# Optimization experiments

Measured on AMD Instinct MI355X. Metric: run time of the kernel, lower is better.

Reference implementation:

```python
import jax, jax.numpy as jnp
import numpy as np

N = 50000
E = 800000
H = 96
NUM_IN = 11
PE_DIM = 24
NUM_OUT = 1
NUM_LAYERS = 4
NUM_GRAPHS = 256


def _linear_params(key, d_in, d_out):
    k1, k2 = jax.random.split(key)
    bound = 1.0 / np.sqrt(d_in)
    w = jax.random.uniform(k1, (d_in, d_out), jnp.float32, -bound, bound)
    b = jax.random.uniform(k2, (d_out,), jnp.float32, -bound, bound)
    return w, b


def setup_inputs() -> dict:
    key = jax.random.key(0)
    ks = jax.random.split(key, 32)
    x = jax.random.normal(ks[0], (N, NUM_IN), jnp.float32)
    pos = jax.random.normal(ks[1], (N, 3), jnp.float32)
    pe = jax.random.normal(ks[2], (N, PE_DIM), jnp.float32)
    edge_index = jax.random.randint(ks[3], (2, E), 0, N, jnp.int64)
    batch = jnp.sort(jax.random.randint(ks[4], (N,), 0, NUM_GRAPHS, jnp.int64))
    embed_w1, embed_b1 = _linear_params(ks[5], NUM_IN + PE_DIM, H)
    embed_w2, embed_b2 = _linear_params(ks[6], H, H)
    # per-layer stacked params
    msg_w1 = []; msg_b1 = []; msg_w2 = []; msg_b2 = []
    upd_w1 = []; upd_b1 = []; upd_w2 = []; upd_b2 = []
    for l in range(NUM_LAYERS):
        w, b = _linear_params(ks[7 + l], 2 * H + 1, H); msg_w1.append(w); msg_b1.append(b)
        w, b = _linear_params(ks[11 + l], H, H); msg_w2.append(w); msg_b2.append(b)
        w, b = _linear_params(ks[15 + l], 2 * H, H); upd_w1.append(w); upd_b1.append(b)
        w, b = _linear_params(ks[19 + l], H, H); upd_w2.append(w); upd_b2.append(b)
    pre_w1, pre_b1 = _linear_params(ks[23], H, H)
    pre_w2, pre_b2 = _linear_params(ks[24], H, H)
    ro_w1, ro_b1 = _linear_params(ks[25], H, H)
    ro_w2, ro_b2 = _linear_params(ks[26], H, NUM_OUT)
    return {
        'x': x, 'pos': pos, 'pe': pe, 'edge_index': edge_index, 'batch': batch,
        'embed_w1': embed_w1, 'embed_b1': embed_b1, 'embed_w2': embed_w2, 'embed_b2': embed_b2,
        'msg_w1': jnp.stack(msg_w1), 'msg_b1': jnp.stack(msg_b1),
        'msg_w2': jnp.stack(msg_w2), 'msg_b2': jnp.stack(msg_b2),
        'upd_w1': jnp.stack(upd_w1), 'upd_b1': jnp.stack(upd_b1),
        'upd_w2': jnp.stack(upd_w2), 'upd_b2': jnp.stack(upd_b2),
        'pre_w1': pre_w1, 'pre_b1': pre_b1, 'pre_w2': pre_w2, 'pre_b2': pre_b2,
        'ro_w1': ro_w1, 'ro_b1': ro_b1, 'ro_w2': ro_w2, 'ro_b2': ro_b2,
    }


def _egnn_forward(x, pos, pe, edge_index, batch,
                  embed_w1, embed_b1, embed_w2, embed_b2,
                  msg_w1, msg_b1, msg_w2, msg_b2,
                  upd_w1, upd_b1, upd_w2, upd_b2,
                  pre_w1, pre_b1, pre_w2, pre_b2,
                  ro_w1, ro_b1, ro_w2, ro_b2):
    silu = jax.nn.silu
    send, rec = edge_index[0], edge_index[1]
    h = jnp.concatenate([x, pe], axis=-1)
    h = silu(h @ embed_w1 + embed_b1) @ embed_w2 + embed_b2  # [N,H]
    dist = jnp.linalg.norm(pos[send] - pos[rec], axis=1)[:, None]  # [E,1]
    for l in range(NUM_LAYERS):
        state = jnp.concatenate([h[send], h[rec], dist], axis=1)  # [E,2H+1]
        msg = silu(silu(state @ msg_w1[l] + msg_b1[l]) @ msg_w2[l] + msg_b2[l])  # [E,H]
        aggr = jax.ops.segment_sum(msg, rec, num_segments=h.shape[0])  # [N,H]
        upd_in = jnp.concatenate([h, aggr], axis=1)
        update = silu(upd_in @ upd_w1[l] + upd_b1[l]) @ upd_w2[l] + upd_b2[l]
        h = h + update
    h = silu(h @ pre_w1 + pre_b1) @ pre_w2 + pre_b2
    pooled = jax.ops.segment_sum(h, batch, num_segments=NUM_GRAPHS)  # [G,H]
    out = silu(pooled @ ro_w1 + ro_b1) @ ro_w2 + ro_b2  # [G,1]
    return jnp.squeeze(out)


def reference(x, pos, pe, edge_index, batch,
              embed_w1, embed_b1, embed_w2, embed_b2,
              msg_w1, msg_b1, msg_w2, msg_b2,
              upd_w1, upd_b1, upd_w2, upd_b2,
              pre_w1, pre_b1, pre_w2, pre_b2,
              ro_w1, ro_b1, ro_w2, ro_b2):
    return _egnn_forward(x, pos, pe, edge_index, batch,
                         embed_w1, embed_b1, embed_w2, embed_b2,
                         msg_w1, msg_b1, msg_w2, msg_b2,
                         upd_w1, upd_b1, upd_w2, upd_b2,
                         pre_w1, pre_b1, pre_w2, pre_b2,
                         ro_w1, ro_b1, ro_w2, ro_b2)
```

## Files before the change

### kernel.cpp

```cpp
#include <hip/hip_runtime.h>
#include <hip/hip_bf16.h>

#define HDIM 96
#define TILE 128
#define NTILE 64

typedef __attribute__((ext_vector_type(8))) short  short8;
typedef __attribute__((ext_vector_type(4))) short  short4v;
typedef __attribute__((ext_vector_type(4))) float  float4v;
typedef __attribute__((ext_vector_type(2))) float  float2v;
typedef __attribute__((ext_vector_type(4))) unsigned int uint4v;
typedef __attribute__((ext_vector_type(2))) unsigned int uint2v;

static __device__ __forceinline__ short f2bf(float f){
    unsigned u = __float_as_uint(f);
    return (short)((u + 0x8000u) >> 16);
}
static __device__ __forceinline__ float bf2f(short s){
    unsigned u = ((unsigned)(unsigned short)s) << 16;
    return __uint_as_float(u);
}
static __device__ __forceinline__ float silu_f(float v){
    return v * __builtin_amdgcn_rcpf(1.0f + __expf(-v));
}
static __device__ __forceinline__ unsigned silu2_pack(float2v v){
    float e0 = __expf(-v[0]);
    float e1 = __expf(-v[1]);
    float2v ep = {e0, e1};
    const float2v one2 = {1.0f, 1.0f};
    ep += one2;
    float2v q = { __builtin_amdgcn_rcpf(ep[0]), __builtin_amdgcn_rcpf(ep[1]) };
    float2v res = v * q;
    unsigned pa = __float_as_uint(res[0]) + 0x8000u;
    unsigned pb = __float_as_uint(res[1]) + 0x8000u;
    return __builtin_amdgcn_perm(pb, pa, 0x07060302);
}

typedef __attribute__((address_space(1))) const unsigned int guint;
typedef __attribute__((address_space(3))) unsigned int luint;
static __device__ __forceinline__ void gload_lds16(const void* g, void* l){
    __builtin_amdgcn_global_load_lds((guint*)g, (luint*)l, 16, 0, 0);
}

struct SwJob { const float* src; int ck; int ks; int ksrc; };
struct SwTable { SwJob j[22]; };

__global__ __launch_bounds__(256) void swizzle_all(SwTable T, const float* __restrict__ msg_w1,
                                                   short* __restrict__ dst, short* __restrict__ dst2,
                                                   int total1, int total2,
                                                   float* __restrict__ aggrZ, float* __restrict__ pooledZ,
                                                   int* __restrict__ degZ, int nA, int nP, int nD){
    int gid = blockIdx.x*256 + threadIdx.x;
    if (gid < total1) {
        int ksg = gid / 3072;
        int e   = gid % 3072;
        const float* src = T.j[0].src; int k0 = 0, ksrc = 0;
        #pragma unroll
        for (int jj = 0; jj < 22; ++jj){
            int s = T.j[jj].ck;
            if (ksg >= s && ksg < s + T.j[jj].ks){ src = T.j[jj].src; k0 = (ksg - s)*32; ksrc = T.j[jj].ksrc; }
        }
        int nt   = e >> 9;
        int rem  = e & 511;
        int lane = rem >> 3;
        int jx   = rem & 7;
        int k = k0 + ((lane >> 4) << 3) + jx;
        int f = nt*16 + (lane & 15);
        float v = (k < ksrc) ? src[(size_t)k*HDIM + f] : 0.0f;
        dst[gid] = f2bf(v);
    } else if (gid < total1 + total2) {
        int g2 = gid - total1;
        int layer = g2 / 18432;
        int e     = g2 % 18432;
        int ksg = e / 6144;
        int rem = e % 6144;
        int nt   = rem >> 9;
        int r2   = rem & 511;
        int lane = r2 >> 3;
        int jx   = r2 & 7;
        int k = ksg*32 + ((lane >> 4) << 3) + jx;
        int f = nt*16 + (lane & 15);
        int row = (f < 96) ? k : (96 + k);
        int col = (f < 96) ? f : (f - 96);
        dst2[g2] = f2bf(msg_w1[(size_t)layer*193*96 + (size_t)row*96 + col]);
    } else {
        int gz = gid - total1 - total2;
        const float4v z = {0.f,0.f,0.f,0.f};
        if (gz < nA)                 ((float4v*)aggrZ)[gz] = z;
        else if (gz < nA + nP)       ((float4v*)pooledZ)[gz - nA] = z;
        else if (gz < nA + nP + nD)  ((float4v*)degZ)[gz - nA - nP] = z;
    }
}

__global__ __launch_bounds__(256) void hist_kernel(const int* __restrict__ rec, int* __restrict__ deg, int E){
    int e = blockIdx.x*256 + threadIdx.x;
    if (e < E) atomicAdd(&deg[rec[e]], 1);
}

__global__ __launch_bounds__(256) void scan_part(const int* __restrict__ deg, int* __restrict__ part, int N){
    __shared__ int red[256];
    const int t = threadIdx.x;
    int base = blockIdx.x*1024;
    int s = 0;
    #pragma unroll
    for (int j=0;j<4;j++){ int i = base + j*256 + t; s += (i<N)?deg[i]:0; }
    red[t]=s; __syncthreads();
    #pragma unroll
    for (int off=128; off>0; off>>=1){ if (t<off) red[t]+=red[t+off]; __syncthreads(); }
    if (t==0) part[blockIdx.x]=red[0];
}
__global__ __launch_bounds__(256) void scan_top(int* __restrict__ part, int nb){
    __shared__ int buf[256];
    const int t = threadIdx.x;
    int v = (t < nb) ? part[t] : 0;
    buf[t] = v;
    __syncthreads();
    #pragma unroll
    for (int off=1; off<256; off<<=1){
        int u = (t>=off)?buf[t-off]:0;
        __syncthreads();
        buf[t] += u;
        __syncthreads();
    }
    if (t < nb) part[t] = buf[t] - v;
}
__global__ __launch_bounds__(256) void scan_final(int* __restrict__ deg, const int* __restrict__ part,
                                                  int* __restrict__ cur, int N){
    __shared__ int tsum[256];
    const int t = threadIdx.x;
    int i0 = blockIdx.x*1024 + t*4;
    int a0 = (i0+0<N)?deg[i0+0]:0;
    int a1 = (i0+1<N)?deg[i0+1]:0;
    int a2 = (i0+2<N)?deg[i0+2]:0;
    int a3 = (i0+3<N)?deg[i0+3]:0;
    int s = a0+a1+a2+a3;
    tsum[t]=s; __syncthreads();
    #pragma unroll
    for (int off=1; off<256; off<<=1){
        int u = (t>=off)?tsum[t-off]:0;
        __syncthreads();
        tsum[t]+=u;
        __syncthreads();
    }
    int excl = tsum[t]-s + part[blockIdx.x];
    int e0 = excl, e1 = excl+a0, e2 = excl+a0+a1, e3 = excl+a0+a1+a2;
    if (i0+0<N){ cur[i0+0]=e0; if (a0>0 && (e0>>7)!=((e0+a0-1)>>7)) deg[i0+0]=a0|0x80000000; }
    if (i0+1<N){ cur[i0+1]=e1; if (a1>0 && (e1>>7)!=((e1+a1-1)>>7)) deg[i0+1]=a1|0x80000000; }
    if (i0+2<N){ cur[i0+2]=e2; if (a2>0 && (e2>>7)!=((e2+a2-1)>>7)) deg[i0+2]=a2|0x80000000; }
    if (i0+3<N){ cur[i0+3]=e3; if (a3>0 && (e3>>7)!=((e3+a3-1)>>7)) deg[i0+3]=a3|0x80000000; }
}

__global__ __launch_bounds__(256) void scatter_kernel(
    const int* __restrict__ send, const int* __restrict__ rec, const float* __restrict__ pos,
    int* __restrict__ cur, int2* __restrict__ sd_s, int* __restrict__ rec_s, int E)
{
    int e = blockIdx.x*256 + threadIdx.x;
    if (e >= E) return;
    int s = send[e], r = rec[e];
    int p = atomicAdd(&cur[r], 1);
    float dx = pos[3*s]   - pos[3*r];
    float dy = pos[3*s+1] - pos[3*r+1];
    float dz = pos[3*s+2] - pos[3*r+2];
    float d = sqrtf(dx*dx + dy*dy + dz*dz);
    sd_s[p] = make_int2(s, __float_as_int(d));
    rec_s[p] = r;
}

template<bool FULL>
static __device__ __forceinline__ void edge_body(
    const short* __restrict__ SR,
    const int2* __restrict__ sd_s, const int* __restrict__ rec_s,
    const float* __restrict__ w1r192,
    const short* __restrict__ w2sw, const float* __restrict__ b2,
    float* __restrict__ aggr, float* __restrict__ stageA, float* __restrict__ stageB, int E,
    short* msgS, int* recS, int* startIdxS, int* wcntS)
{
    const int t  = threadIdx.x;
    const int e0 = blockIdx.x * TILE;
    const int lane = t & 63;
    const int wv   = t >> 6;
    const int e_lo = wv * 32;
    const int col  = lane & 15;
    const int quad = lane >> 4;
    const int frow = quad * 4;
    const float4v fzero = {0.f,0.f,0.f,0.f};
    const int emax = E - 1;

    int seStage[6];
    const int* sdp = (const int*)sd_s;
    #pragma unroll
    for (int i=0;i<6;i++){
        int idx = i*4 + wv;
        int e  = ((idx & 1) << 6) + lane;
        int ec = e0 + e;
        if (!FULL) ec = min(ec, emax);
        seStage[i] = sdp[2*ec];
    }
    #pragma unroll
    for (int i=0;i<6;i++){
        int idx = i*4 + wv;
        int cc  = idx >> 1;
        const short* src = SR + (size_t)seStage[i]*192 + cc*8;
        gload_lds16(src, msgS + idx*512);
    }

    int re[2]; float dd[2];
    #pragma unroll
    for (int et=0; et<2; ++et){
        int ec = e0 + e_lo + et*16 + col;
        if (!FULL) ec = min(ec, emax);
        int2 sd = sd_s[ec];
        dd[et] = __int_as_float(sd.y);
        re[et] = rec_s[ec];
    }
    uint4v Rvu[2][3];
    #pragma unroll
    for (int et=0; et<2; ++et)
      #pragma unroll
      for (int ks=0; ks<3; ++ks){
        int f0 = ks*32 + quad*8;
        Rvu[et][ks] = *(const uint4v*)(SR + (size_t)re[et]*192 + 96 + f0);
      }

    int myRec = 0;
    bool flag = false;
    if (t < TILE) {
        int e = e0 + t;
        if (!FULL) e = min(e, emax);
        myRec = rec_s[e];
        recS[t] = myRec;
        int ep = e0 + t - 1;
        if (!FULL && ep > emax) ep = emax;
        flag = (t == 0) || (myRec != rec_s[ep]);
    }
    unsigned long long bmask = __ballot(flag ? 1 : 0);
    int pre = __popcll(bmask & ((1ull << (t & 63)) - 1ull));
    if (t < TILE && (t & 63) == 0) wcntS[t >> 6] = __popcll(bmask);

    const bool firstB = (e0 > 0) && (rec_s[e0-1] == rec_s[e0]);
    const bool lastB  = (e0 + TILE < E) && (rec_s[e0 + TILE] == rec_s[FULL ? (e0+TILE-1) : min(e0+TILE-1, emax)]);

    __syncthreads();

    if (flag) startIdxS[pre + ((t >> 6) ? wcntS[0] : 0)] = t;
    if (t == 0) startIdxS[wcntS[0] + wcntS[1]] = TILE;

    short8 frag[2][3];
    #pragma unroll
    for (int et=0; et<2; ++et){
        float2v d2 = {dd[et], dd[et]};
        int e_local = e_lo + et*16 + col;
        #pragma unroll
        for (int ks=0; ks<3; ++ks){
            int f0 = ks*32 + quad*8;
            const float2v* wp = (const float2v*)(w1r192 + f0);
            uint4v su = *(const uint4v*)(msgS + (ks*4+quad)*1024 + e_local*8);
            uint4v ru = Rvu[et][ks];
            uint4v fo;
            #pragma unroll
            for (int p=0;p<4;p++){
                float2v w2 = wp[p];
                unsigned us = su[p], ur = ru[p];
                float2v s2 = { __uint_as_float(us << 16), __uint_as_float(us & 0xffff0000u) };
                float2v r2 = { __uint_as_float(ur << 16), __uint_as_float(ur & 0xffff0000u) };
                float2v v = s2 + r2 + d2*w2;
                fo[p] = silu2_pack(v);
            }
            short8 fr;
            __builtin_memcpy(&fr, &fo, 16);
            frag[et][ks] = fr;
        }
    }
    __syncthreads();

    float4v acc2[2][6];
    #pragma unroll
    for (int i=0;i<2;i++)
      #pragma unroll
      for (int n=0;n<6;n++) acc2[i][n] = fzero;

    const short8* w2f = (const short8*)w2sw;
    #pragma unroll
    for (int ks = 0; ks < 3; ++ks) {
        #pragma unroll
        for (int mt = 0; mt < 6; ++mt) {
            short8 a = w2f[(ks*6+mt)*64 + lane];
            acc2[0][mt] = __builtin_amdgcn_mfma_f32_16x16x32_bf16(a, frag[0][ks], acc2[0][mt], 0, 0, 0);
            acc2[1][mt] = __builtin_amdgcn_mfma_f32_16x16x32_bf16(a, frag[1][ks], acc2[1][mt], 0, 0, 0);
        }
    }
    float4v b2v[6];
    #pragma unroll
    for (int mt=0; mt<6; ++mt) b2v[mt] = *(const float4v*)(b2 + mt*16 + frow);

    #pragma unroll
    for (int et=0; et<2; ++et){
        int e = e_lo + et*16 + col;
        bool valid = FULL || ((e0 + e) < E);
        #pragma unroll
        for (int mt=0; mt<6; ++mt){
            float2v aLo = *(const float2v*)&acc2[et][mt];
            float2v aHi = *((const float2v*)&acc2[et][mt] + 1);
            float2v bLo = *(const float2v*)&b2v[mt];
            float2v bHi = *((const float2v*)&b2v[mt] + 1);
            unsigned ulo = silu2_pack(aLo + bLo);
            unsigned uhi = silu2_pack(aHi + bHi);
            if (!valid){ ulo = 0u; uhi = 0u; }
            uint2v st = {ulo, uhi};
            *(uint2v*)(msgS + e*104 + mt*16 + frow) = st;
        }
    }
    __syncthreads();

    const int nseg = wcntS[0] + wcntS[1];
    const int items = nseg * 24;
    for (int item = t; item < items; item += 256){
        int s  = item / 24;
        int fg = item - s*24;
        int r0 = startIdxS[s], r1 = startIdxS[s+1];
        float2v s01 = {0.f,0.f}, s23 = {0.f,0.f};
        for (int r = r0; r < r1; ++r){
            const unsigned* pp = (const unsigned*)(msgS + r*104 + fg*4);
            unsigned p0 = pp[0], p1 = pp[1];
            float2v a0 = { __uint_as_float(p0 << 16), __uint_as_float(p0 & 0xffff0000u) };
            float2v a1 = { __uint_as_float(p1 << 16), __uint_as_float(p1 & 0xffff0000u) };
            s01 += a0; s23 += a1;
        }
        int node = recS[r0];
        float* dstp;
        if (s == 0 && firstB)            dstp = stageB + (size_t)node*HDIM + fg*4;
        else if (s == nseg-1 && lastB)   dstp = stageA + (size_t)node*HDIM + fg*4;
        else                             dstp = aggr   + (size_t)node*HDIM + fg*4;
        float4v v = {s01[0], s01[1], s23[0], s23[1]};
        *(float4v*)(dstp) = v;
    }
}

__global__ __launch_bounds__(256,5) void edge_kernel(
    const short* __restrict__ SR,
    const int2* __restrict__ sd_s, const int* __restrict__ rec_s,
    const float* __restrict__ w1r192,
    const short* __restrict__ w2sw, const float* __restrict__ b2,
    float* __restrict__ aggr, float* __restrict__ stageA, float* __restrict__ stageB, int E)
{
    __shared__ short msgS[TILE*104];
    __shared__ int   recS[TILE];
    __shared__ int   startIdxS[TILE+1];
    __shared__ int   wcntS[2];
    const int e0 = blockIdx.x * TILE;
    if (e0 + TILE <= E)
        edge_body<true >(SR, sd_s, rec_s, w1r192, w2sw, b2, aggr, stageA, stageB, E, msgS, recS, startIdxS, wcntS);
    else
        edge_body<false>(SR, sd_s, rec_s, w1r192, w2sw, b2, aggr, stageA, stageB, E, msgS, recS, startIdxS, wcntS);
}

__global__ __launch_bounds__(256,3) void update_kernel(
    short* __restrict__ hbf, const float* __restrict__ aggr,
    const float* __restrict__ stageA, const float* __restrict__ stageB,
    const int* __restrict__ deg,
    const short* __restrict__ w1sw, const float* __restrict__ b1,
    const short* __restrict__ w2sw, const float* __restrict__ b2,
    const short* __restrict__ w1sr_next, const float* __restrict__ msgb1_next,
    short* __restrict__ SR,
    const short* __restrict__ pw1, const float* __restrict__ pb1,
    const short* __restrict__ pw2, const float* __restrict__ pb2,
    const int* __restrict__ batch, float* __restrict__ pooled, int N)
{
    __shared__ short stateS[NTILE*208];
    __shared__ int   batchS[NTILE];
    __shared__ int   startIdxS[NTILE+1];
    __shared__ int   nsegS;
    const int t  = threadIdx.x;
    const int n0 = blockIdx.x * NTILE;

    #pragma unroll
    for (int it = 0; it < 6; ++it) {
        int q = it*256 + t;
        int c = q % 24;
        int i = q / 24;
        int node = n0 + i;
        if (c < 12) {
            uint4v v = {0u,0u,0u,0u};
            if (node < N) v = *(const uint4v*)(hbf + (size_t)node*HDIM + c*8);
            *(uint4v*)(stateS + i*200 + c*8) = v;
        } else {
            int cc = c - 12;
            short8 s8 = {0,0,0,0,0,0,0,0};
            if (node < N) {
                bool bnd = deg[node] < 0;
                float4v a0, a1;
                if (bnd) {
                    size_t b = (size_t)node*HDIM + cc*8;
                    a0 = *(const float4v*)(stageA + b)     + *(const float4v*)(stageB + b);
                    a1 = *(const float4v*)(stageA + b + 4) + *(const float4v*)(stageB + b + 4);
                } else {
                    a0 = *(const float4v*)(aggr + (size_t)node*HDIM + cc*8);
                    a1 = *(const float4v*)(aggr + (size_t)node*HDIM + cc*8 + 4);
                }
                s8[0]=f2bf(a0[0]); s8[1]=f2bf(a0[1]); s8[2]=f2bf(a0[2]); s8[3]=f2bf(a0[3]);
                s8[4]=f2bf(a1[0]); s8[5]=f2bf(a1[1]); s8[6]=f2bf(a1[2]); s8[7]=f2bf(a1[3]);
            }
            *(short8*)(stateS + i*200 + HDIM + cc*8) = s8;
        }
    }
    __syncthreads();

    const int lane = t & 63;
    const int wv   = t >> 6;
    const int rb   = wv * 16;
    const int col  = lane & 15;
    const int quad = lane >> 4;
    const int koff = quad * 8;
    const int frow = quad * 4;
    const float4v fzero = {0.f,0.f,0.f,0.f};

    float4v acc[6];
    #pragma unroll
    for (int n=0;n<6;n++) acc[n] = fzero;

    const short8* w1f = (const short8*)w1sw;
    #pragma unroll
    for (int ks = 0; ks < 6; ++ks) {
        short8 bb = *(const short8*)(stateS + (rb+col)*200 + ks*32 + koff);
        #pragma unroll
        for (int mt = 0; mt < 6; ++mt) {
            short8 a = w1f[(ks*6+mt)*64 + lane];
            acc[mt] = __builtin_amdgcn_mfma_f32_16x16x32_bf16(a, bb, acc[mt], 0, 0, 0);
        }
    }
    float4v b1v[6];
    #pragma unroll
    for (int mt=0; mt<6; ++mt) b1v[mt] = *(const float4v*)(b1 + mt*16 + frow);
    __syncthreads();

    short* t1S = stateS;
    {
        int e = rb + col;
        #pragma unroll
        for (int mt=0; mt<6; ++mt){
            short4v sv;
            #pragma unroll
            for (int r=0;r<4;r++) sv[r] = f2bf(silu_f(acc[mt][r] + b1v[mt][r]));
            *(short4v*)(t1S + e*104 + mt*16 + frow) = sv;
        }
    }
    __syncthreads();

    float4v acc2[6];
    #pragma unroll
    for (int n=0;n<6;n++) acc2[n] = fzero;

    const short8* w2f = (const short8*)w2sw;
    #pragma unroll
    for (int ks = 0; ks < 3; ++ks) {
        short8 bb = *(const short8*)(t1S + (rb+col)*104 + ks*32 + koff);
        #pragma unroll
        for (int mt = 0; mt < 6; ++mt) {
            short8 a = w2f[(ks*6+mt)*64 + lane];
            acc2[mt] = __builtin_amdgcn_mfma_f32_16x16x32_bf16(a, bb, acc2[mt], 0, 0, 0);
        }
    }
    float4v b2v[6];
    #pragma unroll
    for (int mt=0; mt<6; ++mt) b2v[mt] = *(const float4v*)(b2 + mt*16 + frow);
    __syncthreads();

    {
        int erow = rb + col;
        int node = n0 + erow;
        bool valid = node < N;
        size_t base = (size_t)node*HDIM;
        #pragma unroll
        for (int mt=0; mt<6; ++mt){
            int f0 = mt*16 + frow;
            short4v ov = {0,0,0,0};
            if (valid) ov = *(const short4v*)(hbf + base + f0);
            float4v o;
            #pragma unroll
            for (int r=0;r<4;r++) o[r] = bf2f(ov[r]) + acc2[mt][r] + b2v[mt][r];
            short4v sv = {f2bf(o[0]), f2bf(o[1]), f2bf(o[2]), f2bf(o[3])};
            if (valid) *(short4v*)(hbf + base + f0) = sv;
            *(short4v*)(stateS + erow*104 + f0) = sv;
        }
    }

    if (w1sr_next) {
        __syncthreads();
        float4v accS[12];
        #pragma unroll
        for (int n=0;n<12;n++) accS[n] = fzero;

        const short8* wsf = (const short8*)w1sr_next;
        #pragma unroll
        for (int ks = 0; ks < 3; ++ks) {
            short8 bb = *(const short8*)(stateS + (rb+col)*104 + ks*32 + koff);
            #pragma unroll
            for (int mt = 0; mt < 12; ++mt) {
                short8 a = wsf[(ks*12+mt)*64 + lane];
                accS[mt] = __builtin_amdgcn_mfma_f32_16x16x32_bf16(a, bb, accS[mt], 0, 0, 0);
            }
        }
        float4v bnv[6];
        #pragma unroll
        for (int mt=0; mt<6; ++mt) bnv[mt] = *(const float4v*)(msgb1_next + mt*16 + frow);

        {
            int node = n0 + rb + col;
            if (node < N) {
                size_t sbase = (size_t)node*192;
                #pragma unroll
                for (int mt=0; mt<12; ++mt){
                    float4v o = accS[mt];
                    if (mt < 6) { o[0]+=bnv[mt][0]; o[1]+=bnv[mt][1]; o[2]+=bnv[mt][2]; o[3]+=bnv[mt][3]; }
                    short4v sv = {f2bf(o[0]), f2bf(o[1]), f2bf(o[2]), f2bf(o[3])};
                    *(short4v*)(SR + sbase + mt*16 + frow) = sv;
                }
            }
        }
    } else if (pw1) {
        if (t < NTILE) {
            int node = n0 + t;
            batchS[t] = batch[node < N ? node : N-1];
        }
        __syncthreads();

        bool flag = false;
        if (t < NTILE) flag = (t == 0) || (batchS[t] != batchS[t-1]);
        unsigned long long bm = __ballot(flag ? 1 : 0);
        if (t < NTILE) {
            int pre = __popcll(bm & ((1ull << t) - 1ull));
            if (flag) startIdxS[pre] = t;
            if (t == 0) nsegS = __popcll(bm);
        }

        float4v accp[6];
        #pragma unroll
        for (int n=0;n<6;n++) accp[n] = fzero;

        const short8* pw1f = (const short8*)pw1;
        #pragma unroll
        for (int ks = 0; ks < 3; ++ks) {
            short8 bb = *(const short8*)(stateS + (rb+col)*104 + ks*32 + koff);
            #pragma unroll
            for (int mt = 0; mt < 6; ++mt) {
                short8 a = pw1f[(ks*6+mt)*64 + lane];
                accp[mt] = __builtin_amdgcn_mfma_f32_16x16x32_bf16(a, bb, accp[mt], 0, 0, 0);
            }
        }
        float4v pb1v[6];
        #pragma unroll
        for (int mt=0; mt<6; ++mt) pb1v[mt] = *(const float4v*)(pb1 + mt*16 + frow);

        short* t1p = stateS + NTILE*104;
        {
            int e = rb + col;
            #pragma unroll
            for (int mt=0; mt<6; ++mt){
                short4v sv;
                #pragma unroll
                for (int r=0;r<4;r++) sv[r] = f2bf(silu_f(accp[mt][r] + pb1v[mt][r]));
                *(short4v*)(t1p + e*104 + mt*16 + frow) = sv;
            }
        }
        __syncthreads();

        float4v accq[6];
        #pragma unroll
        for (int n=0;n<6;n++) accq[n] = fzero;

        const short8* pw2f = (const short8*)pw2;
        #pragma unroll
        for (int ks = 0; ks < 3; ++ks) {
            short8 bb = *(const short8*)(t1p + (rb+col)*104 + ks*32 + koff);
            #pragma unroll
            for (int mt = 0; mt < 6; ++mt) {
                short8 a = pw2f[(ks*6+mt)*64 + lane];
                accq[mt] = __builtin_amdgcn_mfma_f32_16x16x32_bf16(a, bb, accq[mt], 0, 0, 0);
            }
        }
        float4v pb2v[6];
        #pragma unroll
        for (int mt=0; mt<6; ++mt) pb2v[mt] = *(const float4v*)(pb2 + mt*16 + frow);
        __syncthreads();

        float* msgS = (float*)stateS;
        {
            int e = rb + col;
            bool valid = (n0 + e) < N;
            #pragma unroll
            for (int mt=0; mt<6; ++mt){
                float4v v;
                #pragma unroll
                for (int r=0;r<4;r++){
                    float u = accq[mt][r] + pb2v[mt][r];
                    v[r] = valid ? u : 0.0f;
                }
                *(float4v*)(msgS + e*100 + mt*16 + frow) = v;
            }
        }
        __syncthreads();

        const int nseg = nsegS;
        if (t == 0) startIdxS[nseg] = NTILE;
        __syncthreads();

        const int items = nseg * 24;
        for (int item = t; item < items; item += 256){
            int s  = item / 24;
            int fg = item - s*24;
            int r0 = startIdxS[s], r1 = startIdxS[s+1];
            float4v sum = fzero;
            for (int r = r0; r < r1; ++r) sum += *(const float4v*)(msgS + r*100 + fg*4);
            float* dstp = pooled + (size_t)batchS[r0]*HDIM + fg*4;
            atomicAdd(dstp+0, sum[0]);
            atomicAdd(dstp+1, sum[1]);
            atomicAdd(dstp+2, sum[2]);
            atomicAdd(dstp+3, sum[3]);
        }
    }
}

__global__ __launch_bounds__(256,3) void embed_kernel(
    const float* __restrict__ x, const float* __restrict__ pe,
    const short* __restrict__ w1sw, const float* __restrict__ b1,
    const short* __restrict__ w2sw, const float* __restrict__ b2,
    short* __restrict__ hbf,
    const short* __restrict__ w1sr0, const float* __restrict__ msgb1_0,
    short* __restrict__ SR, int N)
{
    __shared__ short stateS[NTILE*72];
    __shared__ short t1S[NTILE*104];
    const int t  = threadIdx.x;
    const int n0 = blockIdx.x * NTILE;

    if (t < NTILE) {
        int node = n0 + t;
        short* row = stateS + t*72;
        if (node < N) {
            #pragma unroll
            for (int j=0;j<11;j++) row[j]    = f2bf(x[(size_t)node*11 + j]);
            #pragma unroll
            for (int j=0;j<24;j++) row[11+j] = f2bf(pe[(size_t)node*24 + j]);
            #pragma unroll
            for (int j=35;j<64;j++) row[j] = 0;
        } else {
            #pragma unroll
            for (int j=0;j<64;j++) row[j] = 0;
        }
    }
    __syncthreads();

    const int lane = t & 63;
    const int wv   = t >> 6;
    const int rb   = wv * 16;
    const int col  = lane & 15;
    const int quad = lane >> 4;
    const int koff = quad * 8;
    const int frow = quad * 4;
    const float4v fzero = {0.f,0.f,0.f,0.f};

    float4v acc[6];
    #pragma unroll
    for (int n=0;n<6;n++) acc[n] = fzero;

    const short8* w1f = (const short8*)w1sw;
    #pragma unroll
    for (int ks = 0; ks < 2; ++ks) {
        short8 bb = *(const short8*)(stateS + (rb+col)*72 + ks*32 + koff);
        #pragma unroll
        for (int mt = 0; mt < 6; ++mt) {
            short8 a = w1f[(ks*6+mt)*64 + lane];
            acc[mt] = __builtin_amdgcn_mfma_f32_16x16x32_bf16(a, bb, acc[mt], 0, 0, 0);
        }
    }
    float4v b1v[6];
    #pragma unroll
    for (int mt=0; mt<6; ++mt) b1v[mt] = *(const float4v*)(b1 + mt*16 + frow);

    {
        int e = rb + col;
        #pragma unroll
        for (int mt=0; mt<6; ++mt){
            short4v sv;
            #pragma unroll
            for (int r=0;r<4;r++) sv[r] = f2bf(silu_f(acc[mt][r] + b1v[mt][r]));
            *(short4v*)(t1S + e*104 + mt*16 + frow) = sv;
        }
    }
    __syncthreads();

    float4v acc2[6];
    #pragma unroll
    for (int n=0;n<6;n++) acc2[n] = fzero;

    const short8* w2f = (const short8*)w2sw;
    #pragma unroll
    for (int ks = 0; ks < 3; ++ks) {
        short8 bb = *(const short8*)(t1S + (rb+col)*104 + ks*32 + koff);
        #pragma unroll
        for (int mt = 0; mt < 6; ++mt) {
            short8 a = w2f[(ks*6+mt)*64 + lane];
            acc2[mt] = __builtin_amdgcn_mfma_f32_16x16x32_bf16(a, bb, acc2[mt], 0, 0, 0);
        }
    }
    float4v b2v[6];
    #pragma unroll
    for (int mt=0; mt<6; ++mt) b2v[mt] = *(const float4v*)(b2 + mt*16 + frow);
    __syncthreads();

    {
        int erow = rb + col;
        int node = n0 + erow;
        bool valid = node < N;
        size_t base = (size_t)node*HDIM;
        #pragma unroll
        for (int mt=0; mt<6; ++mt){
            int f0 = mt*16 + frow;
            float4v o;
            #pragma unroll
            for (int r=0;r<4;r++) o[r] = acc2[mt][r] + b2v[mt][r];
            short4v sv = {f2bf(o[0]), f2bf(o[1]), f2bf(o[2]), f2bf(o[3])};
            if (valid) *(short4v*)(hbf + base + f0) = sv;
            *(short4v*)(t1S + erow*104 + f0) = sv;
        }
    }
    __syncthreads();

    float4v accS[12];
    #pragma unroll
    for (int n=0;n<12;n++) accS[n] = fzero;

    const short8* wsf = (const short8*)w1sr0;
    #pragma unroll
    for (int ks = 0; ks < 3; ++ks) {
        short8 bb = *(const short8*)(t1S + (rb+col)*104 + ks*32 + koff);
        #pragma unroll
        for (int mt = 0; mt < 12; ++mt) {
            short8 a = wsf[(ks*12+mt)*64 + lane];
            accS[mt] = __builtin_amdgcn_mfma_f32_16x16x32_bf16(a, bb, accS[mt], 0, 0, 0);
        }
    }
    float4v bnv[6];
    #pragma unroll
    for (int mt=0; mt<6; ++mt) bnv[mt] = *(const float4v*)(msgb1_0 + mt*16 + frow);

    {
        int node = n0 + rb + col;
        if (node < N) {
            size_t sbase = (size_t)node*192;
            #pragma unroll
            for (int mt=0; mt<12; ++mt){
                float4v o = accS[mt];
                if (mt < 6) { o[0]+=bnv[mt][0]; o[1]+=bnv[mt][1]; o[2]+=bnv[mt][2]; o[3]+=bnv[mt][3]; }
                short4v sv = {f2bf(o[0]), f2bf(o[1]), f2bf(o[2]), f2bf(o[3])};
                *(short4v*)(SR + sbase + mt*16 + frow) = sv;
            }
        }
    }
}

__global__ __launch_bounds__(128) void readout_kernel(
    const float* __restrict__ pooled,
    const float* __restrict__ w1, const float* __restrict__ b1,
    const float* __restrict__ w2, const float* __restrict__ b2,
    float* __restrict__ out)
{
    __shared__ float red[128];
    const int g = blockIdx.x;
    const int t = threadIdx.x;
    float p = 0.0f;
    if (t < HDIM) {
        float acc = b1[t];
        for (int k = 0; k < HDIM; ++k)
            acc += pooled[(size_t)g*HDIM + k] * w1[(size_t)k*HDIM + t];
        acc = silu_f(acc);
        p = acc * w2[t];
    }
    red[t] = p;
    __syncthreads();
    for (int s = 64; s > 0; s >>= 1) {
        if (t < s) red[t] += red[t + s];
        __syncthreads();
    }
    if (t == 0) out[g] = red[0] + b2[0];
}

extern "C" void kernel_launch(void* const* d_in, const int* in_sizes, int n_in,
                              void* d_out, int out_size, void* d_ws, size_t ws_size,
                              hipStream_t stream)
{
    const float* x        = (const float*)d_in[0];
    const float* pos      = (const float*)d_in[1];
    const float* pe       = (const float*)d_in[2];
    const int*   ei       = (const int*)d_in[3];
    const int*   batch    = (const int*)d_in[4];
    const float* embed_w1 = (const float*)d_in[5];
    const float* embed_b1 = (const float*)d_in[6];
    const float* embed_w2 = (const float*)d_in[7];
    const float* embed_b2 = (const float*)d_in[8];
    const float* msg_w1   = (const float*)d_in[9];
    const float* msg_b1   = (const float*)d_in[10];
    const float* msg_w2   = (const float*)d_in[11];
    const float* msg_b2   = (const float*)d_in[12];
    const float* upd_w1   = (const float*)d_in[13];
    const float* upd_b1   = (const float*)d_in[14];
    const float* upd_w2   = (const float*)d_in[15];
    const float* upd_b2   = (const float*)d_in[16];
    const float* pre_w1   = (const float*)d_in[17];
    const float* pre_b1   = (const float*)d_in[18];
    const float* pre_w2   = (const float*)d_in[19];
    const float* pre_b2   = (const float*)d_in[20];
    const float* ro_w1    = (const float*)d_in[21];
    const float* ro_b1    = (const float*)d_in[22];
    const float* ro_w2    = (const float*)d_in[23];
    const float* ro_b2    = (const float*)d_in[24];

    const int E = in_sizes[3] / 2;
    const int N = in_sizes[4];
    const int G = out_size;

    char* ws = (char*)d_ws;
    size_t off = 0;
    auto alloc = [&](size_t bytes){ void* p = ws + off; off += (bytes + 255) & ~(size_t)255; return p; };
    short* hbf    = (short*)alloc((size_t)N*HDIM*2);
    float* aggr   = (float*)alloc((size_t)N*HDIM*4);
    float* stageA = (float*)alloc((size_t)N*HDIM*4);
    float* stageB = (float*)alloc((size_t)N*HDIM*4);
    float* pooled = (float*)alloc((size_t)G*HDIM*4);
    short* wsw    = (short*)alloc((size_t)59*3072*2);
    short* w1sr   = (short*)alloc((size_t)4*18432*2);
    short* SR     = (short*)alloc((size_t)N*192*2);
    int*   deg    = (int*)alloc((size_t)N*4);
    int*   cur    = (int*)alloc((size_t)N*4);
    int*   part   = (int*)alloc((size_t)256*4);
    int2*  sd_s   = (int2*)alloc((size_t)E*8);
    int*   rec_s  = (int*)alloc((size_t)E*4);

    SwTable T;
    for (int jj=0;jj<22;jj++){ T.j[jj].src = embed_w1; T.j[jj].ck = 1<<30; T.j[jj].ks = 0; T.j[jj].ksrc = 0; }
    int ck = 0, ji = 0;
    auto add = [&](const float* s, int ks, int ksrc){
        T.j[ji].src = s; T.j[ji].ck = ck; T.j[ji].ks = ks; T.j[ji].ksrc = ksrc;
        ji++; ck += ks;
    };
    add(embed_w1, 2, 35);
    add(embed_w2, 3, 96);
    add(pre_w1,   3, 96);
    add(pre_w2,   3, 96);
    for (int l=0;l<4;l++) add(msg_w2 + (size_t)l*96*96,  3, 96);
    for (int l=0;l<4;l++) add(upd_w1 + (size_t)l*192*96, 6, 192);
    for (int l=0;l<4;l++) add(upd_w2 + (size_t)l*96*96,  3, 96);
    const int total1 = 59*3072;
    const int total2 = 4*18432;
    const int nA = N*24;
    const int nP = G*24;
    const int nD = (N+3)/4;
    const int totalZ = nA + nP + nD;
    swizzle_all<<<(total1+total2+totalZ+255)/256, 256, 0, stream>>>(T, msg_w1, wsw, w1sr, total1, total2,
                                                                   aggr, pooled, deg, nA, nP, nD);

    const int nbE256 = (E + 255) / 256;
    const int nbScan = (N + 1023) / 1024;
    hist_kernel<<<nbE256, 256, 0, stream>>>(ei + E, deg, E);
    scan_part<<<nbScan, 256, 0, stream>>>(deg, part, N);
    scan_top<<<1, 256, 0, stream>>>(part, nbScan);
    scan_final<<<nbScan, 256, 0, stream>>>(deg, part, cur, N);
    scatter_kernel<<<nbE256, 256, 0, stream>>>(ei, ei + E, pos, cur, sd_s, rec_s, E);

    const int nbN = (N + NTILE - 1) / NTILE;
    embed_kernel<<<nbN, 256, 0, stream>>>(x, pe, wsw + 0, embed_b1, wsw + 2*3072, embed_b2,
                                          hbf, w1sr, msg_b1, SR, N);

    const int nbE = (E + TILE - 1) / TILE;
    for (int l = 0; l < 4; ++l) {
        edge_kernel<<<nbE, 256, 0, stream>>>(SR, sd_s, rec_s,
            msg_w1 + (size_t)l*193*96 + (size_t)192*96,
            wsw + (11 + 3*l)*3072, msg_b2 + l*96, aggr, stageA, stageB, E);
        const short* w1sr_next  = (l < 3) ? (w1sr + (size_t)(l+1)*18432) : nullptr;
        const float* msgb1_next = (l < 3) ? (msg_b1 + (l+1)*96) : nullptr;
        const short* pw1 = (l == 3) ? (wsw + 5*3072) : nullptr;
        const float* pb1 = (l == 3) ? pre_b1 : nullptr;
        const short* pw2 = (l == 3) ? (wsw + 8*3072) : nullptr;
        const float* pb2 = (l == 3) ? pre_b2 : nullptr;
        update_kernel<<<nbN, 256, 0, stream>>>(hbf, aggr, stageA, stageB, deg,
            wsw + (23 + 6*l)*3072, upd_b1 + l*96,
            wsw + (47 + 3*l)*3072, upd_b2 + l*96,
            w1sr_next, msgb1_next, SR,
            pw1, pb1, pw2, pb2, batch, pooled, N);
    }

    readout_kernel<<<G, 128, 0, stream>>>(pooled, ro_w1, ro_b1, ro_w2, ro_b2, (float*)d_out);
}
```

Baseline: 711.0 us.

## Load update-kernel MFMA operands directly into registers and drop block barriers

The update kernel no longer stages h and the aggregated messages through shared memory. Each lane loads its own bf16 B-fragments for the first MLP layer straight from global memory into registers. Since every wave now only reads shared-memory rows it wrote itself, several __syncthreads barriers are removed. This cuts LDS traffic and block-level synchronisation, at the cost of less coalesced global loads and higher register pressure. Out-of-range rows are clamped to node N-1 and gated by a valid flag.

```diff
diff --git a/kernel.cpp b/kernel.cpp
--- a/kernel.cpp
+++ b/kernel.cpp
@@ -372,39 +372,6 @@
     __shared__ int   nsegS;
     const int t  = threadIdx.x;
     const int n0 = blockIdx.x * NTILE;
-
-    #pragma unroll
-    for (int it = 0; it < 6; ++it) {
-        int q = it*256 + t;
-        int c = q % 24;
-        int i = q / 24;
-        int node = n0 + i;
-        if (c < 12) {
-            uint4v v = {0u,0u,0u,0u};
-            if (node < N) v = *(const uint4v*)(hbf + (size_t)node*HDIM + c*8);
-            *(uint4v*)(stateS + i*200 + c*8) = v;
-        } else {
-            int cc = c - 12;
-            short8 s8 = {0,0,0,0,0,0,0,0};
-            if (node < N) {
-                bool bnd = deg[node] < 0;
-                float4v a0, a1;
-                if (bnd) {
-                    size_t b = (size_t)node*HDIM + cc*8;
-                    a0 = *(const float4v*)(stageA + b)     + *(const float4v*)(stageB + b);
-                    a1 = *(const float4v*)(stageA + b + 4) + *(const float4v*)(stageB + b + 4);
-                } else {
-                    a0 = *(const float4v*)(aggr + (size_t)node*HDIM + cc*8);
-                    a1 = *(const float4v*)(aggr + (size_t)node*HDIM + cc*8 + 4);
-                }
-                s8[0]=f2bf(a0[0]); s8[1]=f2bf(a0[1]); s8[2]=f2bf(a0[2]); s8[3]=f2bf(a0[3]);
-                s8[4]=f2bf(a1[0]); s8[5]=f2bf(a1[1]); s8[6]=f2bf(a1[2]); s8[7]=f2bf(a1[3]);
-            }
-            *(short8*)(stateS + i*200 + HDIM + cc*8) = s8;
-        }
-    }
-    __syncthreads();
-
     const int lane = t & 63;
     const int wv   = t >> 6;
     const int rb   = wv * 16;
@@ -414,6 +381,35 @@
     const int frow = quad * 4;
     const float4v fzero = {0.f,0.f,0.f,0.f};
 
+    const int nodeRaw = n0 + rb + col;
+    const bool valid  = nodeRaw < N;
+    const int  node   = valid ? nodeRaw : N - 1;
+    const size_t hbase = (size_t)node * HDIM;
+
+    short8 bh[3];
+    #pragma unroll
+    for (int ks=0; ks<3; ++ks)
+        bh[ks] = *(const short8*)(hbf + hbase + ks*32 + koff);
+
+    const bool bnd = deg[node] < 0;
+    short8 ba[3];
+    #pragma unroll
+    for (int ks=0; ks<3; ++ks){
+        size_t b = hbase + ks*32 + koff;
+        float4v a0, a1;
+        if (bnd){
+            a0 = *(const float4v*)(stageA + b)     + *(const float4v*)(stageB + b);
+            a1 = *(const float4v*)(stageA + b + 4) + *(const float4v*)(stageB + b + 4);
+        } else {
+            a0 = *(const float4v*)(aggr + b);
+            a1 = *(const float4v*)(aggr + b + 4);
+        }
+        short8 s8;
+        s8[0]=f2bf(a0[0]); s8[1]=f2bf(a0[1]); s8[2]=f2bf(a0[2]); s8[3]=f2bf(a0[3]);
+        s8[4]=f2bf(a1[0]); s8[5]=f2bf(a1[1]); s8[6]=f2bf(a1[2]); s8[7]=f2bf(a1[3]);
+        ba[ks] = s8;
+    }
+
     float4v acc[6];
     #pragma unroll
     for (int n=0;n<6;n++) acc[n] = fzero;
@@ -421,7 +417,7 @@
     const short8* w1f = (const short8*)w1sw;
     #pragma unroll
     for (int ks = 0; ks < 6; ++ks) {
-        short8 bb = *(const short8*)(stateS + (rb+col)*200 + ks*32 + koff);
+        short8 bb = (ks < 3) ? bh[ks] : ba[ks-3];
         #pragma unroll
         for (int mt = 0; mt < 6; ++mt) {
             short8 a = w1f[(ks*6+mt)*64 + lane];
@@ -431,7 +427,6 @@
     float4v b1v[6];
     #pragma unroll
     for (int mt=0; mt<6; ++mt) b1v[mt] = *(const float4v*)(b1 + mt*16 + frow);
-    __syncthreads();
 
     short* t1S = stateS;
     {
@@ -444,7 +439,6 @@
             *(short4v*)(t1S + e*104 + mt*16 + frow) = sv;
         }
     }
-    __syncthreads();
 
     float4v acc2[6];
     #pragma unroll
@@ -463,12 +457,9 @@
     float4v b2v[6];
     #pragma unroll
     for (int mt=0; mt<6; ++mt) b2v[mt] = *(const float4v*)(b2 + mt*16 + frow);
-    __syncthreads();
 
     {
         int erow = rb + col;
-        int node = n0 + erow;
-        bool valid = node < N;
         size_t base = (size_t)node*HDIM;
         #pragma unroll
         for (int mt=0; mt<6; ++mt){
@@ -485,7 +476,6 @@
     }
 
     if (w1sr_next) {
-        __syncthreads();
         float4v accS[12];
         #pragma unroll
         for (int n=0;n<12;n++) accS[n] = fzero;
@@ -504,23 +494,20 @@
         #pragma unroll
         for (int mt=0; mt<6; ++mt) bnv[mt] = *(const float4v*)(msgb1_next + mt*16 + frow);
 
-        {
-            int node = n0 + rb + col;
-            if (node < N) {
-                size_t sbase = (size_t)node*192;
-                #pragma unroll
-                for (int mt=0; mt<12; ++mt){
-                    float4v o = accS[mt];
-                    if (mt < 6) { o[0]+=bnv[mt][0]; o[1]+=bnv[mt][1]; o[2]+=bnv[mt][2]; o[3]+=bnv[mt][3]; }
-                    short4v sv = {f2bf(o[0]), f2bf(o[1]), f2bf(o[2]), f2bf(o[3])};
-                    *(short4v*)(SR + sbase + mt*16 + frow) = sv;
-                }
+        if (valid) {
+            size_t sbase = (size_t)node*192;
+            #pragma unroll
+            for (int mt=0; mt<12; ++mt){
+                float4v o = accS[mt];
+                if (mt < 6) { o[0]+=bnv[mt][0]; o[1]+=bnv[mt][1]; o[2]+=bnv[mt][2]; o[3]+=bnv[mt][3]; }
+                short4v sv = {f2bf(o[0]), f2bf(o[1]), f2bf(o[2]), f2bf(o[3])};
+                *(short4v*)(SR + sbase + mt*16 + frow) = sv;
             }
         }
     } else if (pw1) {
         if (t < NTILE) {
-            int node = n0 + t;
-            batchS[t] = batch[node < N ? node : N-1];
+            int nd = n0 + t;
+            batchS[t] = batch[nd < N ? nd : N-1];
         }
         __syncthreads();
 
@@ -562,7 +549,6 @@
                 *(short4v*)(t1p + e*104 + mt*16 + frow) = sv;
             }
         }
-        __syncthreads();
 
         float4v accq[6];
         #pragma unroll
@@ -586,7 +572,6 @@
         float* msgS = (float*)stateS;
         {
             int e = rb + col;
-            bool valid = (n0 + e) < N;
             #pragma unroll
             for (int mt=0; mt<6; ++mt){
                 float4v v;
```

After: 673.0 us. -5.3%, faster.
